# Kernel optimization log

Measured on AMD Instinct MI355X. Metric: run time of the kernel, lower is better.

The kernel has to match this reference:

```python
import jax, jax.numpy as jnp
import numpy as np

B, T, E, H = 2, 1024, 1024, 16
D = E // H
HEAVY_RATIO = 0.1
RECENT_RATIO = 0.1
QUANT_RATIO = 0.5  # module-level global `quantized_ratio`
NEG = jnp.finfo(jnp.float32).min


def setup_inputs() -> dict:
    key = jax.random.key(0)
    ks = jax.random.split(key, 10)
    s = 0.02
    hidden_states = jax.random.normal(ks[0], (B, T, E), jnp.float32)
    causal = jnp.tril(jnp.ones((T, T), bool))
    attention_mask = jnp.broadcast_to(jnp.where(causal, 0.0, NEG).astype(jnp.float32)[None, None], (B, 1, T, T))
    lin = lambda k: (jax.random.normal(k, (E, E), jnp.float32) * s)
    return {
        'hidden_states': hidden_states,
        'attention_mask': attention_mask,
        'Wq': lin(ks[1]), 'bq': jnp.zeros((E,), jnp.float32),
        'Wk': lin(ks[2]), 'bk': jnp.zeros((E,), jnp.float32),
        'Wv': lin(ks[3]), 'bv': jnp.zeros((E,), jnp.float32),
        'Wo': lin(ks[4]), 'bo': jnp.zeros((E,), jnp.float32),
    }


def _heavy_hitter_mask(aw, hb):
    # aw: [BH, T, T] masked attn logits. Faithful to local_heavy_hitter_mask
    # (use_gumbel=False path, no padding). Returns bool mask_bottom [BH, T, T].
    BH, Tt, _ = aw.shape
    tmp = jax.nn.softmax(aw, axis=-1)               # fp32 softmax
    acc = tmp[:, :hb, :].sum(axis=1)                # [BH, T]
    acc = acc * (jnp.arange(Tt) < hb)               # zero cols >= hb
    col_lt_hb = (jnp.arange(Tt) < hb)
    init_block = jnp.broadcast_to(col_lt_hb[None, None, :], (BH, hb, Tt))
    row_ids = jnp.arange(BH)[:, None]
    cols = jnp.arange(Tt)

    def step(acc, xs):
        row, t = xs                                  # row: [BH, T], t: scalar index
        tmp_i = jax.nn.softmax(row, axis=-1)
        _, idx = jax.lax.top_k(acc, hb - 1)          # heavy-hitter indices [BH, hb-1]
        mb = jnp.zeros((BH, Tt), bool).at[row_ids, idx].set(True)
        mb = mb | (cols == t)[None, :]               # always keep current token
        acc = (acc + tmp_i) * mb                     # accumulate + evict
        return acc, mb

    ts = jnp.arange(hb, Tt)
    rows = jnp.swapaxes(aw[:, hb:, :], 0, 1)         # [T-hb, BH, T]
    _, mbs = jax.lax.scan(step, acc, (rows, ts))
    mask = jnp.concatenate([init_block, jnp.swapaxes(mbs, 0, 1)], axis=1)
    return jnp.tril(mask)


def reference(hidden_states, attention_mask, Wq, bq, Wk, bk, Wv, bv, Wo, bo):
    scaling = D ** -0.5
    shape = lambda x: jnp.transpose(x.reshape(B, T, H, D), (0, 2, 1, 3)).reshape(B * H, T, D)
    q = shape((hidden_states @ Wq + bq) * scaling)
    k = shape(hidden_states @ Wk + bk)
    v = shape(hidden_states @ Wv + bv)

    aw = jnp.einsum('btd,bsd->bts', q, k)                      # [BH, T, T]
    aw = aw.reshape(B, H, T, T) + attention_mask               # additive causal mask
    aw = jnp.maximum(aw, NEG).reshape(B * H, T, T)

    hb = int(HEAVY_RATIO * T)
    qt = int(hb * QUANT_RATIO)
    hb = hb + qt                                               # inflated heavy budget
    recent = int(RECENT_RATIO * T)

    mask_bottom = _heavy_hitter_mask(jax.lax.stop_gradient(aw), hb)
    recent_mask = jnp.triu(jnp.ones((T, T), bool), -recent)    # recent window
    mask = jnp.tril(mask_bottom | recent_mask[None])

    # torch code recomputes the identical masked logits; reuse aw
    aw = jnp.where(mask, aw, jnp.min(attention_mask))
    probs = jax.nn.softmax(aw, axis=-1)
    out = jnp.einsum('bts,bsd->btd', probs, v)                 # [BH, T, D]
    out = jnp.transpose(out.reshape(B, H, T, D), (0, 2, 1, 3)).reshape(B, T, E)
    return out @ Wo + bo
```

## Files before the change

kernel.cpp:

```cpp
#include <hip/hip_runtime.h>
#include <hip/hip_bf16.h>
#include <stdint.h>

#define TT 1024
#define EE 1024
#define HH 16
#define DD 64
#define BHN 32
#define HB 153
#define RECW 102
#define RING 16
#define INFLT 8
#define NEGF (-3.4028234663852886e38f)

typedef unsigned long long ull;
typedef __attribute__((ext_vector_type(8))) short bf16x8;
typedef __attribute__((ext_vector_type(4))) float f32x4;
typedef __attribute__((address_space(3))) float lds_float;

#define OFF_Q  ((size_t)0)
#define OFF_K  (OFF_Q + (size_t)BHN*TT*DD)
#define OFF_V  (OFF_K + (size_t)BHN*TT*DD)
#define OFF_AW (OFF_V + (size_t)BHN*TT*DD)
#define OFF_M  (OFF_AW + (size_t)BHN*TT*TT)
#define OFF_S  (OFF_M + (size_t)BHN*TT)
#define OFF_AO (OFF_S + (size_t)BHN*TT)
#define OFF_END (OFF_AO + (size_t)BHN*TT*DD)

__device__ __forceinline__ ushort f2bf(float x) {
  unsigned u = __float_as_uint(x);
  u = (u + 0x7FFF + ((u >> 16) & 1)) >> 16;
  return (ushort)u;
}
__device__ __forceinline__ float bf2f(ushort h) {
  return __uint_as_float((unsigned)h << 16);
}

__global__ __launch_bounds__(256) void k_pmm(const float* __restrict__ X,
    const float* __restrict__ W, const float* __restrict__ bias,
    float* __restrict__ Y, float scale, int mode) {
  __shared__ ushort Ah[64][72], Al[64][72];
  __shared__ ushort Bh[64][72], Bl[64][72];
  int tid = threadIdx.x, lane = tid & 63, wid = tid >> 6;
  int r = tid >> 2, c0 = (tid & 3) * 16;
  int r0 = blockIdx.y * 64, n0 = blockIdx.x * 64;

  f32x4 acc[4];
  #pragma unroll
  for (int nc = 0; nc < 4; ++nc) acc[nc] = (f32x4){0.f, 0.f, 0.f, 0.f};

  for (int k0 = 0; k0 < EE; k0 += 64) {
    __syncthreads();
    {
      const float4* xs = (const float4*)(X + (size_t)(r0 + r) * EE + k0 + c0);
      #pragma unroll
      for (int q4 = 0; q4 < 4; ++q4) {
        float4 v = xs[q4];
        float f[4] = {v.x, v.y, v.z, v.w};
        ushort hi[4], lo[4];
        #pragma unroll
        for (int u = 0; u < 4; ++u) {
          hi[u] = f2bf(f[u]);
          lo[u] = f2bf(f[u] - bf2f(hi[u]));
        }
        *(unsigned*)&Ah[r][c0 + q4*4]     = (unsigned)hi[0] | ((unsigned)hi[1] << 16);
        *(unsigned*)&Ah[r][c0 + q4*4 + 2] = (unsigned)hi[2] | ((unsigned)hi[3] << 16);
        *(unsigned*)&Al[r][c0 + q4*4]     = (unsigned)lo[0] | ((unsigned)lo[1] << 16);
        *(unsigned*)&Al[r][c0 + q4*4 + 2] = (unsigned)lo[2] | ((unsigned)lo[3] << 16);
      }
    }
    {
      const float4* wsrc = (const float4*)(W + (size_t)(k0 + r) * EE + n0 + c0);
      #pragma unroll
      for (int q4 = 0; q4 < 4; ++q4) {
        float4 v = wsrc[q4];
        float f[4] = {v.x, v.y, v.z, v.w};
        #pragma unroll
        for (int u = 0; u < 4; ++u) {
          ushort hi = f2bf(f[u]);
          ushort lo = f2bf(f[u] - bf2f(hi));
          int c = c0 + q4*4 + u;
          Bh[c][r] = hi;
          Bl[c][r] = lo;
        }
      }
    }
    __syncthreads();
    #pragma unroll
    for (int kb = 0; kb < 2; ++kb) {
      bf16x8 ah = *(const bf16x8*)&Ah[wid*16 + (lane & 15)][kb*32 + (lane >> 4)*8];
      bf16x8 al = *(const bf16x8*)&Al[wid*16 + (lane & 15)][kb*32 + (lane >> 4)*8];
      #pragma unroll
      for (int nc = 0; nc < 4; ++nc) {
        bf16x8 bh_ = *(const bf16x8*)&Bh[nc*16 + (lane & 15)][kb*32 + (lane >> 4)*8];
        bf16x8 bl_ = *(const bf16x8*)&Bl[nc*16 + (lane & 15)][kb*32 + (lane >> 4)*8];
        acc[nc] = __builtin_amdgcn_mfma_f32_16x16x32_bf16(ah, bh_, acc[nc], 0, 0, 0);
        acc[nc] = __builtin_amdgcn_mfma_f32_16x16x32_bf16(al, bh_, acc[nc], 0, 0, 0);
        acc[nc] = __builtin_amdgcn_mfma_f32_16x16x32_bf16(ah, bl_, acc[nc], 0, 0, 0);
      }
    }
  }

  int rowbase = wid*16 + (lane >> 4)*4;
  #pragma unroll
  for (int nc = 0; nc < 4; ++nc) {
    int c = n0 + nc*16 + (lane & 15);
    float bv = bias[c];
    #pragma unroll
    for (int qq = 0; qq < 4; ++qq) {
      int rr = r0 + rowbase + qq;
      float val = (acc[nc][qq] + bv) * scale;
      int b_ = rr >> 10, t_ = rr & 1023, h_ = c >> 6, d_ = c & 63;
      if (mode == 1) {
        Y[(((size_t)(b_*HH + h_) * TT) + t_) * DD + d_] = val;
      } else if (mode == 2) {
        ((ushort*)Y)[(((size_t)(b_*HH + h_) * TT) + t_) * DD + d_] = f2bf(val);
      } else {
        Y[(size_t)rr * EE + c] = val;
      }
    }
  }
}

__global__ __launch_bounds__(256) void k_qk_mfma(const float* __restrict__ q,
    const float* __restrict__ k, float* __restrict__ aw) {
  int bh = blockIdx.y, tt = blockIdx.x;
  int t0 = tt * 64;
  int tid = threadIdx.x, lane = tid & 63, wid = tid >> 6;
  int r = tid >> 2, c0 = (tid & 3) * 16;
  __shared__ ushort Qh[64][72], Ql[64][72];
  __shared__ ushort Kh[64][72], Kl[64][72];
  const float* qb = q + (size_t)bh * TT * DD;
  const float* kb = k + (size_t)bh * TT * DD;
  float* awb = aw + (size_t)bh * TT * TT;

  {
    const float4* xs = (const float4*)(qb + (size_t)(t0 + r) * DD + c0);
    #pragma unroll
    for (int q4 = 0; q4 < 4; ++q4) {
      float4 v = xs[q4];
      float f[4] = {v.x, v.y, v.z, v.w};
      ushort hi[4], lo[4];
      #pragma unroll
      for (int u = 0; u < 4; ++u) {
        hi[u] = f2bf(f[u]);
        lo[u] = f2bf(f[u] - bf2f(hi[u]));
      }
      *(unsigned*)&Qh[r][c0 + q4*4]     = (unsigned)hi[0] | ((unsigned)hi[1] << 16);
      *(unsigned*)&Qh[r][c0 + q4*4 + 2] = (unsigned)hi[2] | ((unsigned)hi[3] << 16);
      *(unsigned*)&Ql[r][c0 + q4*4]     = (unsigned)lo[0] | ((unsigned)lo[1] << 16);
      *(unsigned*)&Ql[r][c0 + q4*4 + 2] = (unsigned)lo[2] | ((unsigned)lo[3] << 16);
    }
  }

  for (int st = 0; st <= tt; ++st) {
    __syncthreads();
    {
      const float4* xs = (const float4*)(kb + (size_t)(st * 64 + r) * DD + c0);
      #pragma unroll
      for (int q4 = 0; q4 < 4; ++q4) {
        float4 v = xs[q4];
        float f[4] = {v.x, v.y, v.z, v.w};
        ushort hi[4], lo[4];
        #pragma unroll
        for (int u = 0; u < 4; ++u) {
          hi[u] = f2bf(f[u]);
          lo[u] = f2bf(f[u] - bf2f(hi[u]));
        }
        *(unsigned*)&Kh[r][c0 + q4*4]     = (unsigned)hi[0] | ((unsigned)hi[1] << 16);
        *(unsigned*)&Kh[r][c0 + q4*4 + 2] = (unsigned)hi[2] | ((unsigned)hi[3] << 16);
        *(unsigned*)&Kl[r][c0 + q4*4]     = (unsigned)lo[0] | ((unsigned)lo[1] << 16);
        *(unsigned*)&Kl[r][c0 + q4*4 + 2] = (unsigned)lo[2] | ((unsigned)lo[3] << 16);
      }
    }
    __syncthreads();
    f32x4 acc[4];
    #pragma unroll
    for (int nc = 0; nc < 4; ++nc) acc[nc] = (f32x4){0.f, 0.f, 0.f, 0.f};
    #pragma unroll
    for (int kb2 = 0; kb2 < 2; ++kb2) {
      bf16x8 ah = *(const bf16x8*)&Qh[wid*16 + (lane & 15)][kb2*32 + (lane >> 4)*8];
      bf16x8 al = *(const bf16x8*)&Ql[wid*16 + (lane & 15)][kb2*32 + (lane >> 4)*8];
      #pragma unroll
      for (int nc = 0; nc < 4; ++nc) {
        bf16x8 bh_ = *(const bf16x8*)&Kh[nc*16 + (lane & 15)][kb2*32 + (lane >> 4)*8];
        bf16x8 bl_ = *(const bf16x8*)&Kl[nc*16 + (lane & 15)][kb2*32 + (lane >> 4)*8];
        acc[nc] = __builtin_amdgcn_mfma_f32_16x16x32_bf16(ah, bh_, acc[nc], 0, 0, 0);
        acc[nc] = __builtin_amdgcn_mfma_f32_16x16x32_bf16(al, bh_, acc[nc], 0, 0, 0);
        acc[nc] = __builtin_amdgcn_mfma_f32_16x16x32_bf16(ah, bl_, acc[nc], 0, 0, 0);
      }
    }
    int rowbase = wid*16 + (lane >> 4)*4;
    #pragma unroll
    for (int nc = 0; nc < 4; ++nc) {
      int s = st * 64 + nc*16 + (lane & 15);
      #pragma unroll
      for (int qq = 0; qq < 4; ++qq) {
        int t_ = t0 + rowbase + qq;
        awb[(size_t)t_ * TT + s] = acc[nc][qq];
      }
    }
  }
}

__global__ __launch_bounds__(256) void k_softmax(float* __restrict__ aw) {
  int bh = blockIdx.y;
  int wid = threadIdx.x >> 6, lane = threadIdx.x & 63;
  int t = blockIdx.x * 4 + wid;
  float* row = aw + ((size_t)bh * TT + t) * TT;
  float vals[16];
  float m = NEGF;
  #pragma unroll
  for (int i = 0; i < 16; ++i) {
    int j = lane + 64*i;
    vals[i] = (j <= t) ? row[j] : NEGF;
    m = fmaxf(m, vals[i]);
  }
  for (int o = 32; o; o >>= 1) m = fmaxf(m, __shfl_xor(m, o));
  float s = 0.f;
  #pragma unroll
  for (int i = 0; i < 16; ++i) {
    int j = lane + 64*i;
    if (j <= t) { vals[i] = expf(vals[i] - m); s += vals[i]; }
  }
  for (int o = 32; o; o >>= 1) s += __shfl_xor(s, o);
  float inv = 1.0f / s;
  #pragma unroll
  for (int i = 0; i < 16; ++i) {
    int j = lane + 64*i;
    if (j <= t) row[j] = vals[i] * inv;
  }
}

__global__ __launch_bounds__(256) void k_init_acc(const float* __restrict__ p,
    float* __restrict__ initacc) {
  int bh = blockIdx.x;
  int c = threadIdx.x;
  float val = 0.f;
  if (c < HB) {
    const float* pb = p + (size_t)bh * TT * TT;
    for (int i = c; i < HB; ++i)
      val += pb[(size_t)i * TT + c];
  }
  initacc[(size_t)bh * 256 + c] = val;
}

#define DPP_HOP(ctrl)                                                        \
  {                                                                          \
    unsigned tt = (unsigned)__builtin_amdgcn_update_dpp(                     \
        (int)0xFFFFFFFFu, (int)x, (ctrl), 0xF, 0xF, false);                  \
    x = x < tt ? x : tt;                                                     \
  }
__device__ __forceinline__ unsigned wave_min_u32(unsigned x) {
  DPP_HOP(0x111)
  DPP_HOP(0x112)
  DPP_HOP(0x114)
  DPP_HOP(0x118)
  DPP_HOP(0x142)
  DPP_HOP(0x143)
  return (unsigned)__builtin_amdgcn_readlane((int)x, 63);
}

__device__ __forceinline__ void gload_lds16(const float* gsrc, float* ldst) {
  __builtin_amdgcn_global_load_lds(
      (const __attribute__((address_space(1))) unsigned int*)gsrc,
      (__attribute__((address_space(3))) unsigned int*)ldst,
      16, 0, 0);
}

__global__ __launch_bounds__(64) void k_scan(const float* __restrict__ p,
    const float* __restrict__ initacc, int* __restrict__ evict_g) {
  int bh = blockIdx.x;
  int lane = threadIdx.x;
  const float* pb = p + (size_t)bh * TT * TT;
  __shared__ float ring[RING][TT];
  __shared__ int ev[TT];
  for (int i = lane; i < TT; i += 64) ev[i] = 0x7fffffff;

  bool act2 = lane < (HB - 128);
  int col0 = lane, col1 = 64 + lane, col2 = act2 ? (128 + lane) : 0;
  float sc0 = initacc[(size_t)bh * 256 + lane];
  float sc1 = initacc[(size_t)bh * 256 + 64 + lane];
  float sc2 = act2 ? initacc[(size_t)bh * 256 + 128 + lane] : 0.f;

  unsigned ring_base = (unsigned)(size_t)(lds_float*)&ring[0][0];

  #pragma unroll
  for (int r = 0; r < INFLT; ++r) {
    const float* srcrow = pb + (size_t)(HB + r) * TT;
    float* slotbase = ring[(HB + r) & (RING - 1)];
    #pragma unroll
    for (int j = 0; j < 4; ++j)
      gload_lds16(srcrow + j * 256 + lane * 4, slotbase + j * 256);
  }

  for (int t = HB; t < TT; ++t) {
    unsigned sbase = ring_base + (unsigned)((t & (RING - 1)) * (TT * 4));
    unsigned a0 = sbase + (unsigned)col0 * 4;
    unsigned a1 = sbase + (unsigned)col1 * 4;
    unsigned a2 = sbase + (unsigned)col2 * 4;
    unsigned ad = sbase + (unsigned)t * 4;
    float r0, r1, r2, rd;
    asm volatile(
      "s_waitcnt vmcnt(28)\n\t"
      "ds_read_b32 %0, %4\n\t"
      "ds_read_b32 %1, %5\n\t"
      "ds_read_b32 %2, %6\n\t"
      "ds_read_b32 %3, %7"
      : "=&v"(r0), "=&v"(r1), "=&v"(r2), "=&v"(rd)
      : "v"(a0), "v"(a1), "v"(a2), "v"(ad)
      : "memory");
    {
      int rn = t + INFLT;
      int rsrc = rn < TT ? rn : TT - 1;
      const float* srcrow = pb + (size_t)rsrc * TT;
      float* slotbase = ring[rn & (RING - 1)];
      #pragma unroll
      for (int j = 0; j < 4; ++j)
        gload_lds16(srcrow + j * 256 + lane * 4, slotbase + j * 256);
    }
    unsigned b0 = __float_as_uint(sc0);
    unsigned b1 = __float_as_uint(sc1);
    unsigned b2 = act2 ? __float_as_uint(sc2) : 0xFFFFFFFFu;
    unsigned mn = b0 < b1 ? b0 : b1; mn = mn < b2 ? mn : b2;
    unsigned mstar = wave_min_u32(mn);
    unsigned c0k = (b0 == mstar) ? (unsigned)(1023 - col0) : 0xFFFFFFFFu;
    unsigned c1k = (b1 == mstar) ? (unsigned)(1023 - col1) : 0xFFFFFFFFu;
    unsigned c2k = (act2 && b2 == mstar) ? (unsigned)(1023 - col2) : 0xFFFFFFFFu;
    unsigned cm = c0k < c1k ? c0k : c1k; cm = cm < c2k ? cm : c2k;
    int cstar = 1023 - (int)wave_min_u32(cm);
    asm volatile("s_waitcnt lgkmcnt(0)" ::: "memory");
    __builtin_amdgcn_sched_barrier(0);
    if (col0 == cstar) { ev[col0] = t; col0 = t; sc0 = rd; } else sc0 += r0;
    if (col1 == cstar) { ev[col1] = t; col1 = t; sc1 = rd; } else sc1 += r1;
    if (act2) {
      if (col2 == cstar) { ev[col2] = t; col2 = t; sc2 = rd; } else sc2 += r2;
    }
  }

  int4* dst4 = (int4*)(evict_g + (size_t)bh * TT);
  const int4* src4 = (const int4*)ev;
  #pragma unroll
  for (int i = 0; i < 4; ++i) dst4[lane + 64 * i] = src4[lane + 64 * i];
}

__global__ __launch_bounds__(256) void k_pv(const float* __restrict__ p,
    const int* __restrict__ evict_g, const ushort* __restrict__ vbf,
    float* __restrict__ ao) {
  int bh = blockIdx.y, tt = blockIdx.x;
  int tid = threadIdx.x, lane = tid & 63, wid = tid >> 6;
  int t0 = tt * 64;
  __shared__ ushort PA[64][72];
  __shared__ ushort VT[64][72];
  __shared__ float rowsum[64];
  __shared__ int et[TT];
  ((int4*)et)[tid] = ((const int4*)(evict_g + (size_t)bh * TT))[tid];
  if (tid < 64) rowsum[tid] = 0.f;
  const float* pb = p + ((size_t)bh * TT + t0) * TT;
  const ushort* vb = vbf + (size_t)bh * TT * DD;

  f32x4 acc[4];
  #pragma unroll
  for (int nc = 0; nc < 4; ++nc) acc[nc] = (f32x4){0.f, 0.f, 0.f, 0.f};

  int r = tid >> 2;
  int c0 = (tid & 3) * 16;
  int tg = t0 + r;
  __syncthreads();

  for (int st = 0; st <= tt; ++st) {
    const float* prow = pb + (size_t)r * TT + st * 64 + c0;
    float part = 0.f;
    ushort tmp16[16];
    #pragma unroll
    for (int q4 = 0; q4 < 4; ++q4) {
      float4 pv4 = *(const float4*)(prow + q4 * 4);
      float vals[4] = {pv4.x, pv4.y, pv4.z, pv4.w};
      #pragma unroll
      for (int u = 0; u < 4; ++u) {
        int j = st * 64 + c0 + q4 * 4 + u;
        bool allow = (j <= tg) && ((et[j] > tg) || (j + RECW >= tg));
        float mv = allow ? vals[u] : 0.f;
        part += mv;
        tmp16[q4 * 4 + u] = f2bf(mv);
      }
    }
    #pragma unroll
    for (int w2 = 0; w2 < 8; ++w2) {
      unsigned pk = (unsigned)tmp16[w2 * 2] | ((unsigned)tmp16[w2 * 2 + 1] << 16);
      *(unsigned*)&PA[r][c0 + w2 * 2] = pk;
    }
    part += __shfl_xor(part, 1);
    part += __shfl_xor(part, 2);
    if ((tid & 3) == 0) rowsum[r] += part;
    {
      const unsigned* vrow32 = (const unsigned*)(vb + (size_t)(st * 64 + r) * DD + c0);
      #pragma unroll
      for (int u = 0; u < 8; ++u) {
        unsigned vv = vrow32[u];
        VT[c0 + u * 2][r] = (ushort)(vv & 0xFFFF);
        VT[c0 + u * 2 + 1][r] = (ushort)(vv >> 16);
      }
    }
    __syncthreads();
    #pragma unroll
    for (int kb = 0; kb < 2; ++kb) {
      bf16x8 af = *(const bf16x8*)&PA[wid * 16 + (lane & 15)][kb * 32 + (lane >> 4) * 8];
      #pragma unroll
      for (int nc = 0; nc < 4; ++nc) {
        bf16x8 bfr = *(const bf16x8*)&VT[nc * 16 + (lane & 15)][kb * 32 + (lane >> 4) * 8];
        acc[nc] = __builtin_amdgcn_mfma_f32_16x16x32_bf16(af, bfr, acc[nc], 0, 0, 0);
      }
    }
    __syncthreads();
  }

  int b_ = bh >> 4, h_ = bh & 15;
  int rl = wid * 16 + (lane >> 4) * 4;
  #pragma unroll
  for (int nc = 0; nc < 4; ++nc) {
    int d = nc * 16 + (lane & 15);
    #pragma unroll
    for (int qq = 0; qq < 4; ++qq) {
      int rr = rl + qq;
      float outv = acc[nc][qq] / rowsum[rr];
      ao[((size_t)b_ * TT + (t0 + rr)) * EE + h_ * DD + d] = outv;
    }
  }
}

extern "C" void kernel_launch(void* const* d_in, const int* in_sizes, int n_in,
                              void* d_out, int out_size, void* d_ws, size_t ws_size,
                              hipStream_t stream) {
  const float* hs = (const float*)d_in[0];
  const float* Wq = (const float*)d_in[2];
  const float* bq = (const float*)d_in[3];
  const float* Wk = (const float*)d_in[4];
  const float* bk = (const float*)d_in[5];
  const float* Wv = (const float*)d_in[6];
  const float* bv = (const float*)d_in[7];
  const float* Wo = (const float*)d_in[8];
  const float* bo = (const float*)d_in[9];
  float* out = (float*)d_out;

  float* ws = (float*)d_ws;
  float* q  = ws + OFF_Q;
  float* k  = ws + OFF_K;
  float* v  = ws + OFF_V;
  float* aw = ws + OFF_AW;
  float* ao = ws + OFF_AO;
  float* initacc = ws + OFF_END;
  int* evict = (int*)(ws + OFF_END + (size_t)BHN * 256);

  dim3 gproj(16, 32);
  k_pmm<<<gproj, 256, 0, stream>>>(hs, Wq, bq, q, 0.125f, 1);
  k_pmm<<<gproj, 256, 0, stream>>>(hs, Wk, bk, k, 1.0f, 1);
  k_pmm<<<gproj, 256, 0, stream>>>(hs, Wv, bv, v, 1.0f, 2);

  dim3 gqk(16, BHN);
  k_qk_mfma<<<gqk, 256, 0, stream>>>(q, k, aw);

  dim3 grs(TT/4, BHN);
  k_softmax<<<grs, 256, 0, stream>>>(aw);

  k_init_acc<<<BHN, 256, 0, stream>>>(aw, initacc);

  k_scan<<<BHN, 64, 0, stream>>>(aw, initacc, evict);

  dim3 gpv(16, BHN);
  k_pv<<<gpv, 256, 0, stream>>>(aw, evict, (const ushort*)v, ao);

  dim3 gout(16, 32);
  k_pmm<<<gout, 256, 0, stream>>>(ao, Wo, bo, out, 1.0f, 0);
}
```

Measured before the change: 590.2 us.

## Software-pipeline heavy-hitter scan LDS reads and skip tie-break reduction when unique

The sequential eviction scan now issues LDS reads for step t+1 before step t's min-reduction, so LDS latency overlaps the wave reduction. Because the evicted slot is not known in advance, it also reads the diagonal element and substitutes it for the slot that was just replaced. A ballot checks whether the minimum is unique, and only then is the second wave-wide tie-break reduction skipped. This shortens the serial critical path per step at the cost of extra registers and slightly more complex control flow.

```diff
diff --git a/kernel.cpp b/kernel.cpp
--- a/kernel.cpp
+++ b/kernel.cpp
@@ -293,23 +293,46 @@
     for (int j = 0; j < 4; ++j)
       gload_lds16(srcrow + j * 256 + lane * 4, slotbase + j * 256);
   }
-
-  for (int t = HB; t < TT; ++t) {
-    unsigned sbase = ring_base + (unsigned)((t & (RING - 1)) * (TT * 4));
+  float r0, r1, r2, rd, re;
+  {
+    unsigned sbase = ring_base + (unsigned)((HB & (RING - 1)) * (TT * 4));
     unsigned a0 = sbase + (unsigned)col0 * 4;
     unsigned a1 = sbase + (unsigned)col1 * 4;
     unsigned a2 = sbase + (unsigned)col2 * 4;
-    unsigned ad = sbase + (unsigned)t * 4;
-    float r0, r1, r2, rd;
+    unsigned ad = sbase + (unsigned)HB * 4;
+    unsigned ae = sbase + (unsigned)(HB - 1) * 4;
+    asm volatile("s_waitcnt vmcnt(28)");
     asm volatile(
-      "s_waitcnt vmcnt(28)\n\t"
-      "ds_read_b32 %0, %4\n\t"
-      "ds_read_b32 %1, %5\n\t"
-      "ds_read_b32 %2, %6\n\t"
-      "ds_read_b32 %3, %7"
-      : "=&v"(r0), "=&v"(r1), "=&v"(r2), "=&v"(rd)
-      : "v"(a0), "v"(a1), "v"(a2), "v"(ad)
-      : "memory");
+      "ds_read_b32 %0, %5\n\t"
+      "ds_read_b32 %1, %6\n\t"
+      "ds_read_b32 %2, %7\n\t"
+      "ds_read_b32 %3, %8\n\t"
+      "ds_read_b32 %4, %9"
+      : "=&v"(r0), "=&v"(r1), "=&v"(r2), "=&v"(rd), "=&v"(re)
+      : "v"(a0), "v"(a1), "v"(a2), "v"(ad), "v"(ae));
+  }
+  bool e0p = false, e1p = false, e2p = false;
+
+  for (int t = HB; t < TT; ++t) {
+    int tn = (t + 1 < TT) ? (t + 1) : (TT - 1);
+    asm volatile("s_waitcnt vmcnt(24)");
+    float n0, n1, n2, nd, ne;
+    {
+      unsigned sbase = ring_base + (unsigned)((tn & (RING - 1)) * (TT * 4));
+      unsigned a0 = sbase + (unsigned)col0 * 4;
+      unsigned a1 = sbase + (unsigned)col1 * 4;
+      unsigned a2 = sbase + (unsigned)col2 * 4;
+      unsigned ad = sbase + (unsigned)tn * 4;
+      unsigned ae = sbase + (unsigned)t * 4;
+      asm volatile(
+        "ds_read_b32 %0, %5\n\t"
+        "ds_read_b32 %1, %6\n\t"
+        "ds_read_b32 %2, %7\n\t"
+        "ds_read_b32 %3, %8\n\t"
+        "ds_read_b32 %4, %9"
+        : "=&v"(n0), "=&v"(n1), "=&v"(n2), "=&v"(nd), "=&v"(ne)
+        : "v"(a0), "v"(a1), "v"(a2), "v"(ad), "v"(ae));
+    }
     {
       int rn = t + INFLT;
       int rsrc = rn < TT ? rn : TT - 1;
@@ -324,18 +347,35 @@
     unsigned b2 = act2 ? __float_as_uint(sc2) : 0xFFFFFFFFu;
     unsigned mn = b0 < b1 ? b0 : b1; mn = mn < b2 ? mn : b2;
     unsigned mstar = wave_min_u32(mn);
-    unsigned c0k = (b0 == mstar) ? (unsigned)(1023 - col0) : 0xFFFFFFFFu;
-    unsigned c1k = (b1 == mstar) ? (unsigned)(1023 - col1) : 0xFFFFFFFFu;
-    unsigned c2k = (act2 && b2 == mstar) ? (unsigned)(1023 - col2) : 0xFFFFFFFFu;
-    unsigned cm = c0k < c1k ? c0k : c1k; cm = cm < c2k ? cm : c2k;
-    int cstar = 1023 - (int)wave_min_u32(cm);
-    asm volatile("s_waitcnt lgkmcnt(0)" ::: "memory");
+    bool m0 = (b0 == mstar), m1 = (b1 == mstar), m2 = act2 && (b2 == mstar);
+    int lcl = (int)m0 + (int)m1 + (int)m2;
+    ull bal1 = __ballot(lcl >= 1);
+    ull bal2 = __ballot(lcl >= 2);
+    bool e0, e1, e2;
+    if (bal2 == 0 && __popcll(bal1) == 1) {
+      e0 = m0; e1 = m1; e2 = m2;
+    } else {
+      unsigned c0k = m0 ? (unsigned)(1023 - col0) : 0xFFFFFFFFu;
+      unsigned c1k = m1 ? (unsigned)(1023 - col1) : 0xFFFFFFFFu;
+      unsigned c2k = m2 ? (unsigned)(1023 - col2) : 0xFFFFFFFFu;
+      unsigned cm = c0k < c1k ? c0k : c1k; cm = cm < c2k ? cm : c2k;
+      int cstar = 1023 - (int)wave_min_u32(cm);
+      e0 = m0 && (col0 == cstar);
+      e1 = m1 && (col1 == cstar);
+      e2 = m2 && (col2 == cstar);
+    }
+    asm volatile("s_waitcnt lgkmcnt(0)");
     __builtin_amdgcn_sched_barrier(0);
-    if (col0 == cstar) { ev[col0] = t; col0 = t; sc0 = rd; } else sc0 += r0;
-    if (col1 == cstar) { ev[col1] = t; col1 = t; sc1 = rd; } else sc1 += r1;
+    float rr0 = e0p ? re : r0;
+    float rr1 = e1p ? re : r1;
+    float rr2 = e2p ? re : r2;
+    if (e0) { ev[col0] = t; col0 = t; sc0 = rd; } else sc0 += rr0;
+    if (e1) { ev[col1] = t; col1 = t; sc1 = rd; } else sc1 += rr1;
     if (act2) {
-      if (col2 == cstar) { ev[col2] = t; col2 = t; sc2 = rd; } else sc2 += r2;
-    }
+      if (e2) { ev[col2] = t; col2 = t; sc2 = rd; } else sc2 += rr2;
+    }
+    e0p = e0; e1p = e1; e2p = e2;
+    r0 = n0; r1 = n1; r2 = n2; rd = nd; re = ne;
   }
 
   int4* dst4 = (int4*)(evict_g + (size_t)bh * TT);
```

New measurement: 572.2 us. -3.1%, faster.

## Interleave two heads per scan wave and software-pipeline LDS reads

Applied to the files above, without the earlier changes.

Each scan wave now processes two batch-heads at once, so two independent serial dependency chains interleave and hide each other's latency. The LDS reads for step t+1 are issued before step t's argmin, with a fixup that swaps in the diagonal value when a column was just replaced. A fast path skips the second wave reduction when the minimum is unique. The launch shrinks to 16 waves and the ring is made shallower, which lowers parallelism across CUs and leaves less prefetch slack.

```diff
diff --git a/kernel.cpp b/kernel.cpp
--- a/kernel.cpp
+++ b/kernel.cpp
@@ -9,8 +9,8 @@
 #define BHN 32
 #define HB 153
 #define RECW 102
-#define RING 16
-#define INFLT 8
+#define RING2 8
+#define INFLT2 6
 #define NEGF (-3.4028234663852886e38f)
 
 typedef unsigned long long ull;
@@ -270,78 +270,190 @@
 
 __global__ __launch_bounds__(64) void k_scan(const float* __restrict__ p,
     const float* __restrict__ initacc, int* __restrict__ evict_g) {
-  int bh = blockIdx.x;
+  int bhA = blockIdx.x * 2, bhB = bhA + 1;
   int lane = threadIdx.x;
-  const float* pb = p + (size_t)bh * TT * TT;
-  __shared__ float ring[RING][TT];
-  __shared__ int ev[TT];
-  for (int i = lane; i < TT; i += 64) ev[i] = 0x7fffffff;
+  const float* pA = p + (size_t)bhA * TT * TT;
+  const float* pB = p + (size_t)bhB * TT * TT;
+  __shared__ float ringA[RING2][TT];
+  __shared__ float ringB[RING2][TT];
+  __shared__ int evA[TT];
+  __shared__ int evB[TT];
+  for (int i = lane; i < TT; i += 64) { evA[i] = 0x7fffffff; evB[i] = 0x7fffffff; }
 
   bool act2 = lane < (HB - 128);
-  int col0 = lane, col1 = 64 + lane, col2 = act2 ? (128 + lane) : 0;
-  float sc0 = initacc[(size_t)bh * 256 + lane];
-  float sc1 = initacc[(size_t)bh * 256 + 64 + lane];
-  float sc2 = act2 ? initacc[(size_t)bh * 256 + 128 + lane] : 0.f;
-
-  unsigned ring_base = (unsigned)(size_t)(lds_float*)&ring[0][0];
-
-  #pragma unroll
-  for (int r = 0; r < INFLT; ++r) {
-    const float* srcrow = pb + (size_t)(HB + r) * TT;
-    float* slotbase = ring[(HB + r) & (RING - 1)];
-    #pragma unroll
-    for (int j = 0; j < 4; ++j)
-      gload_lds16(srcrow + j * 256 + lane * 4, slotbase + j * 256);
-  }
+  int aC0 = lane, aC1 = 64 + lane, aC2 = act2 ? (128 + lane) : 0;
+  int bC0 = lane, bC1 = 64 + lane, bC2 = act2 ? (128 + lane) : 0;
+  float aS0 = initacc[(size_t)bhA * 256 + lane];
+  float aS1 = initacc[(size_t)bhA * 256 + 64 + lane];
+  float aS2 = act2 ? initacc[(size_t)bhA * 256 + 128 + lane] : 0.f;
+  float bS0 = initacc[(size_t)bhB * 256 + lane];
+  float bS1 = initacc[(size_t)bhB * 256 + 64 + lane];
+  float bS2 = act2 ? initacc[(size_t)bhB * 256 + 128 + lane] : 0.f;
+
+  unsigned baseA = (unsigned)(size_t)(lds_float*)&ringA[0][0];
+  unsigned baseB = (unsigned)(size_t)(lds_float*)&ringB[0][0];
+
+  #pragma unroll
+  for (int r = 0; r < INFLT2; ++r) {
+    const float* sA = pA + (size_t)(HB + r) * TT;
+    float* dA = ringA[(HB + r) & (RING2 - 1)];
+    #pragma unroll
+    for (int j = 0; j < 4; ++j) gload_lds16(sA + j * 256 + lane * 4, dA + j * 256);
+    const float* sB = pB + (size_t)(HB + r) * TT;
+    float* dB = ringB[(HB + r) & (RING2 - 1)];
+    #pragma unroll
+    for (int j = 0; j < 4; ++j) gload_lds16(sB + j * 256 + lane * 4, dB + j * 256);
+  }
+
+  float rA0, rA1, rA2, rAd, rAe, rB0, rB1, rB2, rBd, rBe;
+  {
+    unsigned sA = baseA + (unsigned)((HB & (RING2 - 1)) * (TT * 4));
+    unsigned sB = baseB + (unsigned)((HB & (RING2 - 1)) * (TT * 4));
+    unsigned a0 = sA + (unsigned)aC0 * 4, a1 = sA + (unsigned)aC1 * 4,
+             a2 = sA + (unsigned)aC2 * 4, ad = sA + (unsigned)HB * 4,
+             ae = sA + (unsigned)(HB - 1) * 4;
+    unsigned b0 = sB + (unsigned)bC0 * 4, b1 = sB + (unsigned)bC1 * 4,
+             b2 = sB + (unsigned)bC2 * 4, bd = sB + (unsigned)HB * 4,
+             be = sB + (unsigned)(HB - 1) * 4;
+    asm volatile("s_waitcnt vmcnt(40)");
+    asm volatile(
+      "ds_read_b32 %0, %10\n\t"
+      "ds_read_b32 %1, %11\n\t"
+      "ds_read_b32 %2, %12\n\t"
+      "ds_read_b32 %3, %13\n\t"
+      "ds_read_b32 %4, %14\n\t"
+      "ds_read_b32 %5, %15\n\t"
+      "ds_read_b32 %6, %16\n\t"
+      "ds_read_b32 %7, %17\n\t"
+      "ds_read_b32 %8, %18\n\t"
+      "ds_read_b32 %9, %19"
+      : "=&v"(rA0), "=&v"(rA1), "=&v"(rA2), "=&v"(rAd), "=&v"(rAe),
+        "=&v"(rB0), "=&v"(rB1), "=&v"(rB2), "=&v"(rBd), "=&v"(rBe)
+      : "v"(a0), "v"(a1), "v"(a2), "v"(ad), "v"(ae),
+        "v"(b0), "v"(b1), "v"(b2), "v"(bd), "v"(be));
+  }
+  bool aE0p = false, aE1p = false, aE2p = false;
+  bool bE0p = false, bE1p = false, bE2p = false;
 
   for (int t = HB; t < TT; ++t) {
-    unsigned sbase = ring_base + (unsigned)((t & (RING - 1)) * (TT * 4));
-    unsigned a0 = sbase + (unsigned)col0 * 4;
-    unsigned a1 = sbase + (unsigned)col1 * 4;
-    unsigned a2 = sbase + (unsigned)col2 * 4;
-    unsigned ad = sbase + (unsigned)t * 4;
-    float r0, r1, r2, rd;
-    asm volatile(
-      "s_waitcnt vmcnt(28)\n\t"
-      "ds_read_b32 %0, %4\n\t"
-      "ds_read_b32 %1, %5\n\t"
-      "ds_read_b32 %2, %6\n\t"
-      "ds_read_b32 %3, %7"
-      : "=&v"(r0), "=&v"(r1), "=&v"(r2), "=&v"(rd)
-      : "v"(a0), "v"(a1), "v"(a2), "v"(ad)
-      : "memory");
+    int tn = (t + 1 < TT) ? (t + 1) : (TT - 1);
+    asm volatile("s_waitcnt vmcnt(32)");
+    float nA0, nA1, nA2, nAd, nAe, nB0, nB1, nB2, nBd, nBe;
     {
-      int rn = t + INFLT;
+      unsigned sA = baseA + (unsigned)((tn & (RING2 - 1)) * (TT * 4));
+      unsigned sB = baseB + (unsigned)((tn & (RING2 - 1)) * (TT * 4));
+      unsigned a0 = sA + (unsigned)aC0 * 4, a1 = sA + (unsigned)aC1 * 4,
+               a2 = sA + (unsigned)aC2 * 4, ad = sA + (unsigned)tn * 4,
+               ae = sA + (unsigned)t * 4;
+      unsigned b0 = sB + (unsigned)bC0 * 4, b1 = sB + (unsigned)bC1 * 4,
+               b2 = sB + (unsigned)bC2 * 4, bd = sB + (unsigned)tn * 4,
+               be = sB + (unsigned)t * 4;
+      asm volatile(
+        "ds_read_b32 %0, %10\n\t"
+        "ds_read_b32 %1, %11\n\t"
+        "ds_read_b32 %2, %12\n\t"
+        "ds_read_b32 %3, %13\n\t"
+        "ds_read_b32 %4, %14\n\t"
+        "ds_read_b32 %5, %15\n\t"
+        "ds_read_b32 %6, %16\n\t"
+        "ds_read_b32 %7, %17\n\t"
+        "ds_read_b32 %8, %18\n\t"
+        "ds_read_b32 %9, %19"
+        : "=&v"(nA0), "=&v"(nA1), "=&v"(nA2), "=&v"(nAd), "=&v"(nAe),
+          "=&v"(nB0), "=&v"(nB1), "=&v"(nB2), "=&v"(nBd), "=&v"(nBe)
+        : "v"(a0), "v"(a1), "v"(a2), "v"(ad), "v"(ae),
+          "v"(b0), "v"(b1), "v"(b2), "v"(bd), "v"(be));
+    }
+    {
+      int rn = t + INFLT2;
       int rsrc = rn < TT ? rn : TT - 1;
-      const float* srcrow = pb + (size_t)rsrc * TT;
-      float* slotbase = ring[rn & (RING - 1)];
-      #pragma unroll
-      for (int j = 0; j < 4; ++j)
-        gload_lds16(srcrow + j * 256 + lane * 4, slotbase + j * 256);
-    }
-    unsigned b0 = __float_as_uint(sc0);
-    unsigned b1 = __float_as_uint(sc1);
-    unsigned b2 = act2 ? __float_as_uint(sc2) : 0xFFFFFFFFu;
-    unsigned mn = b0 < b1 ? b0 : b1; mn = mn < b2 ? mn : b2;
-    unsigned mstar = wave_min_u32(mn);
-    unsigned c0k = (b0 == mstar) ? (unsigned)(1023 - col0) : 0xFFFFFFFFu;
-    unsigned c1k = (b1 == mstar) ? (unsigned)(1023 - col1) : 0xFFFFFFFFu;
-    unsigned c2k = (act2 && b2 == mstar) ? (unsigned)(1023 - col2) : 0xFFFFFFFFu;
-    unsigned cm = c0k < c1k ? c0k : c1k; cm = cm < c2k ? cm : c2k;
-    int cstar = 1023 - (int)wave_min_u32(cm);
-    asm volatile("s_waitcnt lgkmcnt(0)" ::: "memory");
+      const float* sA = pA + (size_t)rsrc * TT;
+      float* dA = ringA[rn & (RING2 - 1)];
+      #pragma unroll
+      for (int j = 0; j < 4; ++j) gload_lds16(sA + j * 256 + lane * 4, dA + j * 256);
+      const float* sB = pB + (size_t)rsrc * TT;
+      float* dB = ringB[rn & (RING2 - 1)];
+      #pragma unroll
+      for (int j = 0; j < 4; ++j) gload_lds16(sB + j * 256 + lane * 4, dB + j * 256);
+    }
+    unsigned aB0 = __float_as_uint(aS0);
+    unsigned aB1 = __float_as_uint(aS1);
+    unsigned aB2 = act2 ? __float_as_uint(aS2) : 0xFFFFFFFFu;
+    unsigned bB0 = __float_as_uint(bS0);
+    unsigned bB1 = __float_as_uint(bS1);
+    unsigned bB2 = act2 ? __float_as_uint(bS2) : 0xFFFFFFFFu;
+    unsigned aMn = aB0 < aB1 ? aB0 : aB1; aMn = aMn < aB2 ? aMn : aB2;
+    unsigned bMn = bB0 < bB1 ? bB0 : bB1; bMn = bMn < bB2 ? bMn : bB2;
+    unsigned aMst = wave_min_u32(aMn);
+    unsigned bMst = wave_min_u32(bMn);
+    bool aM0 = (aB0 == aMst), aM1 = (aB1 == aMst), aM2 = act2 && (aB2 == aMst);
+    bool bM0 = (bB0 == bMst), bM1 = (bB1 == bMst), bM2 = act2 && (bB2 == bMst);
+    int aL = (int)aM0 + (int)aM1 + (int)aM2;
+    int bL = (int)bM0 + (int)bM1 + (int)bM2;
+    ull aBal1 = __ballot(aL >= 1), aBal2 = __ballot(aL >= 2);
+    ull bBal1 = __ballot(bL >= 1), bBal2 = __ballot(bL >= 2);
+    bool aE0, aE1, aE2, bE0, bE1, bE2;
+    if (aBal2 == 0 && __popcll(aBal1) == 1) {
+      aE0 = aM0; aE1 = aM1; aE2 = aM2;
+    } else {
+      unsigned c0k = aM0 ? (unsigned)(1023 - aC0) : 0xFFFFFFFFu;
+      unsigned c1k = aM1 ? (unsigned)(1023 - aC1) : 0xFFFFFFFFu;
+      unsigned c2k = aM2 ? (unsigned)(1023 - aC2) : 0xFFFFFFFFu;
+      unsigned cm = c0k < c1k ? c0k : c1k; cm = cm < c2k ? cm : c2k;
+      int cstar = 1023 - (int)wave_min_u32(cm);
+      aE0 = aM0 && (aC0 == cstar);
+      aE1 = aM1 && (aC1 == cstar);
+      aE2 = aM2 && (aC2 == cstar);
+    }
+    if (bBal2 == 0 && __popcll(bBal1) == 1) {
+      bE0 = bM0; bE1 = bM1; bE2 = bM2;
+    } else {
+      unsigned c0k = bM0 ? (unsigned)(1023 - bC0) : 0xFFFFFFFFu;
+      unsigned c1k = bM1 ? (unsigned)(1023 - bC1) : 0xFFFFFFFFu;
+      unsigned c2k = bM2 ? (unsigned)(1023 - bC2) : 0xFFFFFFFFu;
+      unsigned cm = c0k < c1k ? c0k : c1k; cm = cm < c2k ? cm : c2k;
+      int cstar = 1023 - (int)wave_min_u32(cm);
+      bE0 = bM0 && (bC0 == cstar);
+      bE1 = bM1 && (bC1 == cstar);
+      bE2 = bM2 && (bC2 == cstar);
+    }
+    asm volatile("s_waitcnt lgkmcnt(10)");
     __builtin_amdgcn_sched_barrier(0);
-    if (col0 == cstar) { ev[col0] = t; col0 = t; sc0 = rd; } else sc0 += r0;
-    if (col1 == cstar) { ev[col1] = t; col1 = t; sc1 = rd; } else sc1 += r1;
+    float pA0 = aE0p ? rAe : rA0;
+    float pA1 = aE1p ? rAe : rA1;
+    float pA2 = aE2p ? rAe : rA2;
+    float pB0 = bE0p ? rBe : rB0;
+    float pB1 = bE1p ? rBe : rB1;
+    float pB2 = bE2p ? rBe : rB2;
+    if (aE0) { evA[aC0] = t; aC0 = t; aS0 = rAd; } else aS0 += pA0;
+    if (aE1) { evA[aC1] = t; aC1 = t; aS1 = rAd; } else aS1 += pA1;
     if (act2) {
-      if (col2 == cstar) { ev[col2] = t; col2 = t; sc2 = rd; } else sc2 += r2;
-    }
-  }
-
-  int4* dst4 = (int4*)(evict_g + (size_t)bh * TT);
-  const int4* src4 = (const int4*)ev;
-  #pragma unroll
-  for (int i = 0; i < 4; ++i) dst4[lane + 64 * i] = src4[lane + 64 * i];
+      if (aE2) { evA[aC2] = t; aC2 = t; aS2 = rAd; } else aS2 += pA2;
+    }
+    if (bE0) { evB[bC0] = t; bC0 = t; bS0 = rBd; } else bS0 += pB0;
+    if (bE1) { evB[bC1] = t; bC1 = t; bS1 = rBd; } else bS1 += pB1;
+    if (act2) {
+      if (bE2) { evB[bC2] = t; bC2 = t; bS2 = rBd; } else bS2 += pB2;
+    }
+    __builtin_amdgcn_sched_barrier(0);
+    aE0p = aE0; aE1p = aE1; aE2p = aE2;
+    bE0p = bE0; bE1p = bE1; bE2p = bE2;
+    rA0 = nA0; rA1 = nA1; rA2 = nA2; rAd = nAd; rAe = nAe;
+    rB0 = nB0; rB1 = nB1; rB2 = nB2; rBd = nBd; rBe = nBe;
+  }
+
+  asm volatile("s_waitcnt lgkmcnt(0)");
+  {
+    int4* dA = (int4*)(evict_g + (size_t)bhA * TT);
+    int4* dB = (int4*)(evict_g + (size_t)bhB * TT);
+    const int4* sA = (const int4*)evA;
+    const int4* sB = (const int4*)evB;
+    #pragma unroll
+    for (int i = 0; i < 4; ++i) {
+      dA[lane + 64 * i] = sA[lane + 64 * i];
+      dB[lane + 64 * i] = sB[lane + 64 * i];
+    }
+  }
 }
 
 __global__ __launch_bounds__(256) void k_pv(const float* __restrict__ p,
@@ -465,7 +577,7 @@
 
   k_init_acc<<<BHN, 256, 0, stream>>>(aw, initacc);
 
-  k_scan<<<BHN, 64, 0, stream>>>(aw, initacc, evict);
+  k_scan<<<BHN/2, 64, 0, stream>>>(aw, initacc, evict);
 
   dim3 gpv(16, BHN);
   k_pv<<<gpv, 256, 0, stream>>>(aw, evict, (const ushort*)v, ao);
```

After: 766.2 us. 1.3x slower.
